# Kernel tuning notes

Hardware: AMD Instinct MI355X
Metric: run time of the kernel (lower is better)

Reference implementation:

```python
import jax, jax.numpy as jnp
import numpy as np

N = 50000        # points
NN = 32          # neighbors per point
K = 15           # kernel points (KPConv default)
D_IN = 64        # backbone channels
D_OUT = 1024     # feeds Linear(1024, 512)
B = 16           # point clouds in the batch
SIGMA = 0.3      # kernel influence radius


def setup_inputs() -> dict:
    key = jax.random.key(0)
    ks = jax.random.split(key, 12)
    pos = jax.random.normal(ks[0], (N, 3), jnp.float32)
    feats = jax.random.normal(ks[1], (N, D_IN), jnp.float32)
    # kernel points roughly inside the influence sphere
    kernel_points = jax.random.normal(ks[2], (K, 3), jnp.float32) * 0.2
    kp_weights = jax.random.normal(ks[3], (K, D_IN, D_OUT), jnp.float32) / np.sqrt(K * D_IN)
    w1 = jax.random.normal(ks[4], (1024, 512), jnp.float32) / np.sqrt(1024)
    b1 = jnp.zeros((512,), jnp.float32)
    w2 = jax.random.normal(ks[5], (512, 256), jnp.float32) / np.sqrt(512)
    b2 = jnp.zeros((256,), jnp.float32)
    w3 = jax.random.normal(ks[6], (256, 152), jnp.float32) / np.sqrt(256)
    b3 = jnp.zeros((152,), jnp.float32)
    neighbor_idx = jax.random.randint(ks[7], (N, NN), 0, N, jnp.int32)
    batch = jnp.sort(jax.random.randint(ks[8], (N,), 0, B, jnp.int32))
    return {"pos": pos, "feats": feats, "kernel_points": kernel_points,
            "kp_weights": kp_weights, "w1": w1, "b1": b1, "w2": w2, "b2": b2,
            "w3": w3, "b3": b3, "neighbor_idx": neighbor_idx, "batch": batch}


def reference(pos, feats, kernel_points, kp_weights, w1, b1, w2, b2, w3, b3,
              neighbor_idx, batch):
    # --- KPConv: gather neighbors, kernel-point correlation, aggregate ---
    rel = pos[neighbor_idx] - pos[:, None, :]                 # [N, NN, 3]
    # distance of each relative neighbor position to each kernel point
    d = jnp.linalg.norm(rel[:, :, None, :] - kernel_points[None, None], axis=-1)  # [N, NN, K]
    h = jnp.maximum(0.0, 1.0 - d / SIGMA)                     # linear correlation
    nbr_f = feats[neighbor_idx]                               # [N, NN, D_IN] gather
    g = jnp.einsum('njk,njd->nkd', h, nbr_f)                  # per-kernel aggregate
    x = jnp.einsum('nkd,kdo->no', g, kp_weights)              # [N, D_OUT]
    x = jax.nn.leaky_relu(x, 0.1)
    # --- global_mean_pool over batch ids ---
    pooled_sum = jax.ops.segment_sum(x, batch, num_segments=B)            # [B, D_OUT]
    counts = jax.ops.segment_sum(jnp.ones((x.shape[0], 1), x.dtype), batch,
                                 num_segments=B)
    pooled = pooled_sum / jnp.maximum(counts, 1.0)
    h1 = jax.nn.relu(pooled @ w1 + b1)
    h2 = jax.nn.relu(h1 @ w2 + b2)
    return h2 @ w3 + b3                                        # [B, 152]
```

## Files before the change

kernel.cpp:

```cpp
#include <hip/hip_runtime.h>
#include <hip/hip_bf16.h>

#define N_PTS 50000
#define NNB   32
#define KP    15
#define DIN   64
#define DOUT  1024
#define KDIM  (KP*DIN)
#define NB    16
#define SIGMA_INV (1.0f/0.3f)

#define BM 64
#define BN 64
#define BK 64
#define NKT (KDIM/BK)
#define RB_FULL 784
#define NCB (DOUT/BN)
#define NWG (RB_FULL*NCB)
#define NSEG 196
#define WT_BLOCKS 240

typedef __attribute__((ext_vector_type(8))) short bf16x8;
typedef __attribute__((ext_vector_type(4))) float f32x4;

#define GLD16(gsrc, ldst) \
  __builtin_amdgcn_global_load_lds((const __attribute__((address_space(1))) char*)(gsrc), \
                                   (__attribute__((address_space(3))) char*)(ldst), 16, 0, 0)

__global__ __launch_bounds__(256) void prep_kernel(
    const float* __restrict__ W, __hip_bfloat16* __restrict__ Wt,
    const float* __restrict__ pos, const float* __restrict__ feats,
    const float* __restrict__ kpts, const int* __restrict__ nidx,
    __hip_bfloat16* __restrict__ g, int* __restrict__ flag,
    int* __restrict__ bcnt) {
  __shared__ union {
    float t[64][65];
    struct { float h[4][16][33]; int cnts; } kc;
  } sm;
  int tid = threadIdx.x;
  if (blockIdx.x < WT_BLOCKS) {
    int i = blockIdx.x;
    int k0 = (i % 15) * 64;
    int o0 = (i / 15) * 64;
    int tx = tid & 63, ty = tid >> 6;
    for (int r = ty; r < 64; r += 4) sm.t[r][tx] = W[(size_t)(k0 + r)*DOUT + o0 + tx];
    __syncthreads();
    for (int r = ty; r < 64; r += 4)
      Wt[(size_t)(o0 + r)*KDIM + k0 + tx] = __float2bfloat16(sm.t[tx][r]);
    return;
  }
  int w = tid >> 6, lane = tid & 63;
  if (tid == 0) sm.kc.cnts = 0;
  __syncthreads();
  int n = (blockIdx.x - WT_BLOCKS) * 4 + w;
  if (n < N_PTS) {
    int myj = lane & 31;
    int khalf = lane >> 5;
    int id0 = nidx[n*NNB + myj];
    float px = pos[n*3+0], py = pos[n*3+1], pz = pos[n*3+2];
    float rx = pos[id0*3+0] - px;
    float ry = pos[id0*3+1] - py;
    float rz = pos[id0*3+2] - pz;
    bool anyact = false;
    float hreg[8];
    #pragma unroll
    for (int i = 0; i < 8; ++i) {
      int k = 2*i + khalf;
      float h = 0.0f;
      if (k < KP) {
        float dx = rx - kpts[k*3+0];
        float dy = ry - kpts[k*3+1];
        float dz = rz - kpts[k*3+2];
        float d = sqrtf(dx*dx + dy*dy + dz*dz);
        h = 1.0f - d * SIGMA_INV;
        h = h > 0.0f ? h : 0.0f;
        anyact |= (h > 0.0f);
      }
      hreg[i] = h;
    }
    unsigned long long bal = __ballot(anyact);
    if (bal) {
      unsigned int actj = (unsigned int)(bal | (bal >> 32));
      if ((actj >> myj) & 1) {
        #pragma unroll
        for (int i = 0; i < 8; ++i) {
          int k = 2*i + khalf;
          if (k < KP) sm.kc.h[w][k][myj] = hreg[i];
        }
      }
      float acc[KP];
      #pragma unroll
      for (int k = 0; k < KP; ++k) acc[k] = 0.0f;
      while (actj) {
        int j = __ffs(actj) - 1;
        actj &= actj - 1;
        int id = __shfl(id0, j);
        float f = feats[(size_t)id*DIN + lane];
        #pragma unroll
        for (int k = 0; k < KP; ++k) acc[k] += sm.kc.h[w][k][j] * f;
      }
      size_t base = (size_t)n*KDIM;
      #pragma unroll
      for (int k = 0; k < KP; ++k)
        g[base + k*DIN + lane] = __float2bfloat16(acc[k]);
    }
    if (lane == 0) {
      int active = (bal != 0ull) ? 1 : 0;
      flag[n] = active;
      if (active) atomicAdd(&sm.kc.cnts, 1);
    }
  }
  __syncthreads();
  if (tid == 0 && sm.kc.cnts) atomicAdd(&bcnt[(blockIdx.x - WT_BLOCKS) >> 6], sm.kc.cnts);
}

__global__ __launch_bounds__(256) void fill_kernel(
    const int* __restrict__ flag, const int* __restrict__ bcnt,
    const int* __restrict__ batch, int* __restrict__ rowlist,
    int* __restrict__ bidc, int* __restrict__ mact) {
  __shared__ int s[256];
  __shared__ int boff_l;
  int tid = threadIdx.x;
  int bc = (tid < NSEG) ? bcnt[tid] : 0;
  s[tid] = (tid < (int)blockIdx.x) ? bc : 0;
  __syncthreads();
  for (int d = 1; d < 256; d <<= 1) {
    int v = (tid >= d) ? s[tid-d] : 0;
    __syncthreads();
    s[tid] += v;
    __syncthreads();
  }
  if (tid == 255) boff_l = s[255];
  __syncthreads();
  int boff = boff_l;
  int n = blockIdx.x*256 + tid;
  int f = (n < N_PTS) ? flag[n] : 0;
  s[tid] = f;
  __syncthreads();
  for (int d = 1; d < 256; d <<= 1) {
    int v = (tid >= d) ? s[tid-d] : 0;
    __syncthreads();
    s[tid] += v;
    __syncthreads();
  }
  if (f) {
    int sl = boff + s[tid] - 1;
    rowlist[sl] = n;
    bidc[sl] = batch[n];
  }
  if (blockIdx.x == NSEG-1 && tid == 255) *mact = boff + s[255];
}

__global__ __launch_bounds__(256) void gemm_mfma_pool(
    const __hip_bfloat16* __restrict__ g, const __hip_bfloat16* __restrict__ Wt,
    const int* __restrict__ rowlist, const int* __restrict__ bidc,
    const int* __restrict__ mact, float* __restrict__ partial) {
  __shared__ __align__(16) char lA[BM*128];
  __shared__ __align__(16) char lB[BN*128];
  __shared__ float psum[NB][BN];
  __shared__ int bid[BM];
  int wg = blockIdx.x;
  int xg = wg & 7, t = wg >> 3;
  int rb = ((t >> 4) << 3) + xg;
  int cb = t & 15;
  int Ma = *mact;
  int r0 = rb*BM, c0 = cb*BN;
  int tid = threadIdx.x;
  if (r0 >= Ma) return;
  int lane = tid & 63, w = tid >> 6;
  int wr = w >> 1, wc = w & 1;

  int gc = (tid & 7) ^ ((tid >> 3) & 7);
  const __hip_bfloat16* pA[2];
  #pragma unroll
  for (int i = 0; i < 2; ++i) {
    int slot = r0 + i*32 + (tid >> 3);
    int rl = (slot < Ma) ? rowlist[slot] : 0;
    pA[i] = g + (size_t)rl*KDIM + gc*8;
  }
  const __hip_bfloat16* pB[2];
  #pragma unroll
  for (int i = 0; i < 2; ++i)
    pB[i] = Wt + (size_t)(c0 + i*32 + (tid >> 3))*KDIM + gc*8;

  if (tid < BM) bid[tid] = (r0 + tid < Ma) ? bidc[r0 + tid] : -1;
  for (int z = tid; z < NB*BN; z += 256) (&psum[0][0])[z] = 0.0f;

  f32x4 acc[2][2] = {};

  for (int kt = 0; kt < NKT; ++kt) {
    int k0 = kt*BK;
    #pragma unroll
    for (int i = 0; i < 2; ++i) GLD16(pA[i] + k0, lA + (i*256 + tid)*16);
    #pragma unroll
    for (int i = 0; i < 2; ++i) GLD16(pB[i] + k0, lB + (i*256 + tid)*16);
    __syncthreads();
    #pragma unroll
    for (int ks = 0; ks < 2; ++ks) {
      bf16x8 af[2], bfr[2];
      #pragma unroll
      for (int m = 0; m < 2; ++m) {
        int row = wr*32 + m*16 + (lane & 15);
        int ch = (ks*4 + (lane >> 4)) ^ (row & 7);
        af[m] = *(const bf16x8*)(lA + row*128 + ch*16);
      }
      #pragma unroll
      for (int n = 0; n < 2; ++n) {
        int row = wc*32 + n*16 + (lane & 15);
        int ch = (ks*4 + (lane >> 4)) ^ (row & 7);
        bfr[n] = *(const bf16x8*)(lB + row*128 + ch*16);
      }
      #pragma unroll
      for (int m = 0; m < 2; ++m)
        #pragma unroll
        for (int n = 0; n < 2; ++n)
          acc[m][n] = __builtin_amdgcn_mfma_f32_16x16x32_bf16(af[m], bfr[n], acc[m][n], 0, 0, 0);
    }
    __syncthreads();
  }

  int q = lane >> 4;
  #pragma unroll 1
  for (int phase = 0; phase < 8; ++phase) {
    if (wr*4 + q == phase) {
      #pragma unroll
      for (int n = 0; n < 2; ++n) {
        int c = wc*32 + n*16 + (lane & 15);
        float run = 0.0f; int curb = -2;
        #pragma unroll
        for (int m = 0; m < 2; ++m) {
          #pragma unroll
          for (int j = 0; j < 4; ++j) {
            int r = wr*32 + m*16 + q*4 + j;
            int b = bid[r];
            float v = acc[m][n][j];
            v = v > 0.0f ? v : 0.1f*v;
            if (b != curb) { if (curb >= 0) psum[curb][c] += run; run = 0.0f; curb = b; }
            run += v;
          }
        }
        if (curb >= 0) psum[curb][c] += run;
      }
    }
    __syncthreads();
  }
  for (int z = tid; z < NB*BN; z += 256) {
    int b = z >> 6, c = z & 63;
    partial[((size_t)rb*NB + b)*DOUT + c0 + c] = psum[b][c];
  }
}

__global__ __launch_bounds__(512) void mlpA_kernel(
    const float* __restrict__ partial, const int* __restrict__ batch,
    const int* __restrict__ mact, const float* __restrict__ w1,
    float* __restrict__ part1) {
  __shared__ float red[16][128];
  __shared__ float pl[128];
  __shared__ float h1p[4][512];
  int s = blockIdx.x, b = blockIdx.y, t = threadIdx.x;
  int nact = (*mact + BM - 1) / BM;
  {
    int seg = t >> 5, q = t & 31;
    float4 v = {0.f, 0.f, 0.f, 0.f};
    for (int rb = seg; rb < nact; rb += 16) {
      const float4 p = *(const float4*)&partial[((size_t)rb*NB + b)*DOUT + s*128 + q*4];
      v.x += p.x; v.y += p.y; v.z += p.z; v.w += p.w;
    }
    *(float4*)&red[seg][q*4] = v;
  }
  __syncthreads();
  if (t < 128) {
    float sum = 0.0f;
    #pragma unroll
    for (int e = 0; e < 16; ++e) sum += red[e][t];
    int lb, ub;
    { int l = 0, r = N_PTS; while (l < r) { int m = (l+r)>>1; if (batch[m] <  b) l = m+1; else r = m; } lb = l; }
    { int l = 0, r = N_PTS; while (l < r) { int m = (l+r)>>1; if (batch[m] <= b) l = m+1; else r = m; } ub = l; }
    pl[t] = sum / fmaxf((float)(ub - lb), 1.0f);
  }
  __syncthreads();
  {
    int oq = t & 127, kseg = t >> 7;
    float4 a = {0.f, 0.f, 0.f, 0.f};
    #pragma unroll 8
    for (int i = 0; i < 32; ++i) {
      int k = kseg*32 + i;
      float p = pl[k];
      const float4 wv = *(const float4*)&w1[(size_t)(s*128 + k)*512 + oq*4];
      a.x += p*wv.x; a.y += p*wv.y; a.z += p*wv.z; a.w += p*wv.w;
    }
    *(float4*)&h1p[kseg][oq*4] = a;
  }
  __syncthreads();
  float r1 = (h1p[0][t] + h1p[1][t]) + (h1p[2][t] + h1p[3][t]);
  part1[((size_t)b*8 + s)*512 + t] = r1;
}

__global__ __launch_bounds__(512) void mlpBC_kernel(
    const float* __restrict__ part1, const float* __restrict__ b1,
    const float* __restrict__ w2, const float* __restrict__ b2,
    const float* __restrict__ w3, const float* __restrict__ b3,
    float* __restrict__ out) {
  __shared__ float hs[512];
  __shared__ float h2p[8][256];
  __shared__ float h2l[256];
  __shared__ float o3p[8][152];
  int b = blockIdx.x, t = threadIdx.x;
  {
    float v = b1[t];
    #pragma unroll
    for (int s = 0; s < 8; ++s) v += part1[((size_t)b*8 + s)*512 + t];
    hs[t] = fmaxf(v, 0.0f);
  }
  __syncthreads();
  {
    int oq = t & 63, kseg = t >> 6;
    float4 a = {0.f, 0.f, 0.f, 0.f};
    #pragma unroll 8
    for (int i = 0; i < 64; ++i) {
      int j = kseg*64 + i;
      float p = hs[j];
      const float4 wv = *(const float4*)&w2[(size_t)j*256 + oq*4];
      a.x += p*wv.x; a.y += p*wv.y; a.z += p*wv.z; a.w += p*wv.w;
    }
    *(float4*)&h2p[kseg][oq*4] = a;
  }
  __syncthreads();
  if (t < 256) {
    float v = b2[t];
    #pragma unroll
    for (int e = 0; e < 8; ++e) v += h2p[e][t];
    h2l[t] = fmaxf(v, 0.0f);
  }
  __syncthreads();
  if (t < 304) {
    int oq = t % 38, kseg = t / 38;
    float4 a = {0.f, 0.f, 0.f, 0.f};
    #pragma unroll 8
    for (int i = 0; i < 32; ++i) {
      int j = kseg*32 + i;
      float p = h2l[j];
      const float4 wv = *(const float4*)&w3[(size_t)j*152 + oq*4];
      a.x += p*wv.x; a.y += p*wv.y; a.z += p*wv.z; a.w += p*wv.w;
    }
    *(float4*)&o3p[kseg][oq*4] = a;
  }
  __syncthreads();
  if (t < 152) {
    float v = b3[t];
    #pragma unroll
    for (int e = 0; e < 8; ++e) v += o3p[e][t];
    out[b*152 + t] = v;
  }
}

extern "C" void kernel_launch(void* const* d_in, const int* in_sizes, int n_in,
                              void* d_out, int out_size, void* d_ws, size_t ws_size,
                              hipStream_t stream) {
  (void)in_sizes; (void)n_in; (void)out_size; (void)ws_size;
  const float* pos   = (const float*)d_in[0];
  const float* feats = (const float*)d_in[1];
  const float* kpts  = (const float*)d_in[2];
  const float* kpw   = (const float*)d_in[3];
  const float* w1    = (const float*)d_in[4];
  const float* b1    = (const float*)d_in[5];
  const float* w2    = (const float*)d_in[6];
  const float* b2    = (const float*)d_in[7];
  const float* w3    = (const float*)d_in[8];
  const float* b3    = (const float*)d_in[9];
  const int* nidx    = (const int*)d_in[10];
  const int* batch   = (const int*)d_in[11];
  float* out = (float*)d_out;

  char* ws = (char*)d_ws;
  const size_t off_g        = 0;
  const size_t off_bidc     = 96000000;
  const size_t off_rowlist  = off_bidc + 200704;
  const size_t off_flag     = off_rowlist + 200704;
  const size_t off_bcnt     = off_flag + 200704;
  const size_t off_mact     = off_bcnt + 1024;
  const size_t off_wt       = off_mact + 64;
  const size_t off_partial  = off_wt + 1966080;
  const size_t off_p1       = off_partial + 51380224;
  __hip_bfloat16* g  = (__hip_bfloat16*)(ws + off_g);
  int* bidc    = (int*)(ws + off_bidc);
  int* rowlist = (int*)(ws + off_rowlist);
  int* flag    = (int*)(ws + off_flag);
  int* bcnt    = (int*)(ws + off_bcnt);
  int* mact    = (int*)(ws + off_mact);
  __hip_bfloat16* wt = (__hip_bfloat16*)(ws + off_wt);
  float* partial = (float*)(ws + off_partial);
  float* part1   = (float*)(ws + off_p1);

  hipMemsetAsync(bcnt, 0, 1024, stream);
  prep_kernel<<<WT_BLOCKS + (N_PTS+3)/4, 256, 0, stream>>>(
      kpw, wt, pos, feats, kpts, nidx, g, flag, bcnt);
  fill_kernel<<<NSEG, 256, 0, stream>>>(flag, bcnt, batch, rowlist, bidc, mact);
  gemm_mfma_pool<<<NWG, 256, 0, stream>>>(g, wt, rowlist, bidc, mact, partial);
  mlpA_kernel<<<dim3(8, NB), 512, 0, stream>>>(partial, batch, mact, w1, part1);
  mlpBC_kernel<<<NB, 512, 0, stream>>>(part1, b1, w2, b2, w3, b3, out);
}
```

Baseline: 152.5 us.

## Sort active rows by kernel-point mask and skip inactive K tiles in GEMM

Each active point now records a 15-bit mask of which kernel points have nonzero correlation. A hash-based counting sort (histogram, scan, scatter kernels) groups rows with similar masks, and the GEMM loops only over K tiles in the OR of its 64 rows' masks. This skips the MFMA work and loads for all-zero kernel-point slices of g. The cost is three extra small kernel launches and more workspace, and the gain depends on how sparse the masks are.

```diff
diff --git a/kernel.cpp b/kernel.cpp
--- a/kernel.cpp
+++ b/kernel.cpp
@@ -27,12 +27,14 @@
   __builtin_amdgcn_global_load_lds((const __attribute__((address_space(1))) char*)(gsrc), \
                                    (__attribute__((address_space(3))) char*)(ldst), 16, 0, 0)
 
+#define MHASH(m) ((int)((((unsigned)(m)) * 2654435761u) >> 24))
+
 __global__ __launch_bounds__(256) void prep_kernel(
     const float* __restrict__ W, __hip_bfloat16* __restrict__ Wt,
     const float* __restrict__ pos, const float* __restrict__ feats,
     const float* __restrict__ kpts, const int* __restrict__ nidx,
     __hip_bfloat16* __restrict__ g, int* __restrict__ flag,
-    int* __restrict__ bcnt) {
+    int* __restrict__ maskArr, int* __restrict__ bcnt) {
   __shared__ union {
     float t[64][65];
     struct { float h[4][16][33]; int cnts; } kc;
@@ -79,6 +81,7 @@
       hreg[i] = h;
     }
     unsigned long long bal = __ballot(anyact);
+    int kb = 0;
     if (bal) {
       unsigned int actj = (unsigned int)(bal | (bal >> 32));
       if ((actj >> myj) & 1) {
@@ -97,7 +100,11 @@
         int id = __shfl(id0, j);
         float f = feats[(size_t)id*DIN + lane];
         #pragma unroll
-        for (int k = 0; k < KP; ++k) acc[k] += sm.kc.h[w][k][j] * f;
+        for (int k = 0; k < KP; ++k) {
+          float hv = sm.kc.h[w][k][j];
+          acc[k] += hv * f;
+          kb |= (hv > 0.0f) ? (1 << k) : 0;
+        }
       }
       size_t base = (size_t)n*KDIM;
       #pragma unroll
@@ -107,7 +114,7 @@
     if (lane == 0) {
       int active = (bal != 0ull) ? 1 : 0;
       flag[n] = active;
-      if (active) atomicAdd(&sm.kc.cnts, 1);
+      if (active) { maskArr[n] = kb; atomicAdd(&sm.kc.cnts, 1); }
     }
   }
   __syncthreads();
@@ -116,8 +123,9 @@
 
 __global__ __launch_bounds__(256) void fill_kernel(
     const int* __restrict__ flag, const int* __restrict__ bcnt,
-    const int* __restrict__ batch, int* __restrict__ rowlist,
-    int* __restrict__ bidc, int* __restrict__ mact) {
+    const int* __restrict__ batch, const int* __restrict__ maskArr,
+    int* __restrict__ rowlist, int* __restrict__ bidc,
+    int* __restrict__ cmask, int* __restrict__ mact) {
   __shared__ int s[256];
   __shared__ int boff_l;
   int tid = threadIdx.x;
@@ -147,18 +155,79 @@
     int sl = boff + s[tid] - 1;
     rowlist[sl] = n;
     bidc[sl] = batch[n];
+    cmask[sl] = maskArr[n];
   }
   if (blockIdx.x == NSEG-1 && tid == 255) *mact = boff + s[255];
+}
+
+__global__ __launch_bounds__(256) void histk_kernel(
+    const int* __restrict__ cmask, const int* __restrict__ mact,
+    int* __restrict__ hist) {
+  __shared__ int h[256];
+  int tid = threadIdx.x;
+  h[tid] = 0;
+  __syncthreads();
+  int Ma = *mact;
+  int slot = blockIdx.x*256 + tid;
+  if (slot < Ma) atomicAdd(&h[MHASH(cmask[slot])], 1);
+  __syncthreads();
+  hist[blockIdx.x*256 + tid] = h[tid];
+}
+
+__global__ __launch_bounds__(256) void scank_kernel(
+    const int* __restrict__ hist, int* __restrict__ off) {
+  __shared__ int s[256];
+  int t = threadIdx.x;
+  int tot = 0;
+  #pragma unroll 7
+  for (int g2 = 0; g2 < NSEG; ++g2) tot += hist[g2*256 + t];
+  s[t] = tot;
+  __syncthreads();
+  for (int d = 1; d < 256; d <<= 1) {
+    int v = (t >= d) ? s[t-d] : 0;
+    __syncthreads();
+    s[t] += v;
+    __syncthreads();
+  }
+  int run = s[t] - tot;
+  #pragma unroll 7
+  for (int g2 = 0; g2 < NSEG; ++g2) { off[g2*256 + t] = run; run += hist[g2*256 + t]; }
+}
+
+__global__ __launch_bounds__(256) void scatk_kernel(
+    const int* __restrict__ cmask, const int* __restrict__ rowlist,
+    const int* __restrict__ bidc, const int* __restrict__ mact,
+    const int* __restrict__ off, int* __restrict__ rl2,
+    int* __restrict__ bd2, int* __restrict__ cm2) {
+  __shared__ int kk[256];
+  int tid = threadIdx.x;
+  int Ma = *mact;
+  int slot = blockIdx.x*256 + tid;
+  int valid = slot < Ma;
+  int cm = valid ? cmask[slot] : 0;
+  int key = valid ? MHASH(cm) : -1;
+  kk[tid] = key;
+  __syncthreads();
+  if (valid) {
+    int lr = 0;
+    for (int j = 0; j < tid; ++j) lr += (kk[j] == key) ? 1 : 0;
+    int pos = off[blockIdx.x*256 + key] + lr;
+    rl2[pos] = rowlist[slot];
+    bd2[pos] = bidc[slot];
+    cm2[pos] = cm;
+  }
 }
 
 __global__ __launch_bounds__(256) void gemm_mfma_pool(
     const __hip_bfloat16* __restrict__ g, const __hip_bfloat16* __restrict__ Wt,
     const int* __restrict__ rowlist, const int* __restrict__ bidc,
-    const int* __restrict__ mact, float* __restrict__ partial) {
+    const int* __restrict__ cmask, const int* __restrict__ mact,
+    float* __restrict__ partial) {
   __shared__ __align__(16) char lA[BM*128];
   __shared__ __align__(16) char lB[BN*128];
   __shared__ float psum[NB][BN];
   __shared__ int bid[BM];
+  __shared__ int mbuf[64];
   int wg = blockIdx.x;
   int xg = wg & 7, t = wg >> 3;
   int rb = ((t >> 4) << 3) + xg;
@@ -183,12 +252,26 @@
   for (int i = 0; i < 2; ++i)
     pB[i] = Wt + (size_t)(c0 + i*32 + (tid >> 3))*KDIM + gc*8;
 
-  if (tid < BM) bid[tid] = (r0 + tid < Ma) ? bidc[r0 + tid] : -1;
+  if (tid < BM) {
+    int s2 = r0 + tid;
+    bid[tid]  = (s2 < Ma) ? bidc[s2] : -1;
+    mbuf[tid] = (s2 < Ma) ? cmask[s2] : 0;
+  }
   for (int z = tid; z < NB*BN; z += 256) (&psum[0][0])[z] = 0.0f;
+  __syncthreads();
+  if (tid == 0) {
+    int m = 0;
+    #pragma unroll
+    for (int i = 0; i < 64; ++i) m |= mbuf[i];
+    mbuf[0] = m;
+  }
+  __syncthreads();
+  unsigned rm = (unsigned)mbuf[0];
 
   f32x4 acc[2][2] = {};
 
-  for (int kt = 0; kt < NKT; ++kt) {
+  while (rm) {
+    int kt = __ffs(rm) - 1; rm &= rm - 1;
     int k0 = kt*BK;
     #pragma unroll
     for (int i = 0; i < 2; ++i) GLD16(pA[i] + k0, lA + (i*256 + tid)*16);
@@ -379,7 +462,14 @@
   const size_t off_flag     = off_rowlist + 200704;
   const size_t off_bcnt     = off_flag + 200704;
   const size_t off_mact     = off_bcnt + 1024;
-  const size_t off_wt       = off_mact + 64;
+  const size_t off_maskA    = off_mact + 64;
+  const size_t off_cmask    = off_maskA + 200704;
+  const size_t off_rl2      = off_cmask + 200704;
+  const size_t off_bd2      = off_rl2 + 200704;
+  const size_t off_cm2      = off_bd2 + 200704;
+  const size_t off_hist     = off_cm2 + 200704;
+  const size_t off_off      = off_hist + 200704;
+  const size_t off_wt       = off_off + 200704;
   const size_t off_partial  = off_wt + 1966080;
   const size_t off_p1       = off_partial + 51380224;
   __hip_bfloat16* g  = (__hip_bfloat16*)(ws + off_g);
@@ -388,15 +478,25 @@
   int* flag    = (int*)(ws + off_flag);
   int* bcnt    = (int*)(ws + off_bcnt);
   int* mact    = (int*)(ws + off_mact);
+  int* maskA   = (int*)(ws + off_maskA);
+  int* cmask   = (int*)(ws + off_cmask);
+  int* rl2     = (int*)(ws + off_rl2);
+  int* bd2     = (int*)(ws + off_bd2);
+  int* cm2     = (int*)(ws + off_cm2);
+  int* hist    = (int*)(ws + off_hist);
+  int* offb    = (int*)(ws + off_off);
   __hip_bfloat16* wt = (__hip_bfloat16*)(ws + off_wt);
   float* partial = (float*)(ws + off_partial);
   float* part1   = (float*)(ws + off_p1);
 
   hipMemsetAsync(bcnt, 0, 1024, stream);
   prep_kernel<<<WT_BLOCKS + (N_PTS+3)/4, 256, 0, stream>>>(
-      kpw, wt, pos, feats, kpts, nidx, g, flag, bcnt);
-  fill_kernel<<<NSEG, 256, 0, stream>>>(flag, bcnt, batch, rowlist, bidc, mact);
-  gemm_mfma_pool<<<NWG, 256, 0, stream>>>(g, wt, rowlist, bidc, mact, partial);
+      kpw, wt, pos, feats, kpts, nidx, g, flag, maskA, bcnt);
+  fill_kernel<<<NSEG, 256, 0, stream>>>(flag, bcnt, batch, maskA, rowlist, bidc, cmask, mact);
+  histk_kernel<<<NSEG, 256, 0, stream>>>(cmask, mact, hist);
+  scank_kernel<<<1, 256, 0, stream>>>(hist, offb);
+  scatk_kernel<<<NSEG, 256, 0, stream>>>(cmask, rowlist, bidc, mact, offb, rl2, bd2, cm2);
+  gemm_mfma_pool<<<NWG, 256, 0, stream>>>(g, wt, rl2, bd2, cm2, mact, partial);
   mlpA_kernel<<<dim3(8, NB), 512, 0, stream>>>(partial, batch, mact, w1, part1);
   mlpBC_kernel<<<NB, 512, 0, stream>>>(part1, b1, w2, b2, w3, b3, out);
 }
```

Measured after the change: 178.0 us. +16.7%, slower.
